# Performance work log

Measured on AMD Instinct MI355X. Metric: run time of the kernel, lower is better.

## Reference

```python
import jax, jax.numpy as jnp
import numpy as np

B, N, K, TC = 4, 4096, 16, 3
N_TAYLOR = 20  # 3rd-order Taylor monomials of (x,y,z): 1 + 3 + 6 + 10
CHANNELS = [(6, 32), (32, 64), (64, 128), (128, 256)]


def _taylor(rel):
    # rel: B,3,N,K relative coords -> B,20,N,K monomial basis up to degree 3
    x, y, z = rel[:, 0], rel[:, 1], rel[:, 2]
    one = jnp.ones_like(x)
    return jnp.stack([one, x, y, z,
                      x * x, x * y, x * z, y * y, y * z, z * z,
                      x * x * x, x * x * y, x * x * z, x * y * y, x * y * z,
                      x * z * z, y * y * y, y * y * z, y * z * z, z * z * z], axis=1)


def _group(feat, idx):
    # feat: B,C,N ; idx: B,N,K (int) -> B,C,N,K gathered neighbor features
    return jax.vmap(lambda f, i: f[:, i])(feat, idx)


def setup_inputs() -> dict:
    key = jax.random.key(0)
    ks = jax.random.split(key, 8)
    inp = {"pc": jax.random.normal(ks[0], (B, N, 6), dtype=jnp.float32)}
    for l, (cin, cout) in enumerate(CHANNELS, start=1):
        k1, k2 = jax.random.split(ks[l], 2)
        inp[f"w1_{l}"] = jax.random.normal(k1, (TC, N_TAYLOR), dtype=jnp.float32) * 0.1
        inp[f"b1_{l}"] = jnp.zeros((TC,), dtype=jnp.float32)
        fan_in = cin * TC * K
        inp[f"w2_{l}"] = jax.random.normal(k2, (cout, cin * TC, K), dtype=jnp.float32) * (1.0 / np.sqrt(fan_in))
        inp[f"b2_{l}"] = jnp.zeros((cout,), dtype=jnp.float32)
    return inp


def _forward(pc, params):
    pcT = pc.transpose(0, 2, 1)                 # B,6,N
    xyz = pcT[:, :3]                            # B,3,N
    # KNN graph: pairwise squared distances, top-k nearest (includes self)
    sq = jnp.sum(xyz * xyz, axis=1)             # B,N
    d2 = sq[:, :, None] + sq[:, None, :] - 2.0 * jnp.einsum('bcn,bcm->bnm', xyz, xyz)
    _, idx = jax.lax.top_k(-d2, K)              # B,N,K
    gxyz = _group(xyz, idx)                     # B,3,N,K
    rel = gxyz - xyz[:, :, :, None]             # B,3,N,K relative neighbor coords
    tay_basis = _taylor(rel)                    # B,20,N,K

    feat = pcT
    feats = []
    for (w1, b1, w2, b2) in params:
        # Taylor kernel weights: 1x1 conv over the 20 monomials -> TC channels
        tay = jnp.einsum('btnk,ct->bcnk', tay_basis, w1) + b1[None, :, None, None]  # B,TC,N,K
        gf = _group(feat, idx)                  # B,C,N,K
        C = gf.shape[1]
        fused = (gf[:, :, None] * tay[:, None]).reshape(B, C * TC, N, K)  # outer product
        # Conv2d(C*TC, out, kernel=(1,K)): contract channel and neighbor axes
        out = jnp.einsum('bcnk,ock->bon', fused, w2) + b2[None, :, None]
        feat = jax.nn.relu(out)                 # B,Cout,N
        feats.append(feat)

    point_feat = jnp.concatenate(feats, axis=1)  # B,480,N
    top2, _ = jax.lax.top_k(point_feat, 2)       # top-2 over N (last axis) -> B,480,2
    cat_feat = top2.reshape(B, -1)               # B,960
    return cat_feat, point_feat


def reference(pc, w1_1, b1_1, w2_1, b2_1, w1_2, b1_2, w2_2, b2_2,
              w1_3, b1_3, w2_3, b2_3, w1_4, b1_4, w2_4, b2_4):
    params = [(w1_1, b1_1, w2_1, b2_1), (w1_2, b1_2, w2_2, b2_2),
              (w1_3, b1_3, w2_3, b2_3), (w1_4, b1_4, w2_4, b2_4)]
    return _forward(pc, params)
```

## Files before the change

### kernel.cpp

```cpp
#include <hip/hip_runtime.h>
#include <hip/hip_fp16.h>
#include <cfloat>

#define BB 4
#define NN 4096
#define KK 16
#define NPTS (BB * NN)
#define NT48 (48 * NPTS)

typedef __attribute__((ext_vector_type(8))) _Float16 f16x8;
typedef __attribute__((ext_vector_type(4))) float f32x4;
typedef unsigned int u32;
typedef unsigned long long u64;

__device__ __forceinline__ short f2h(float v) {
  __half h = __float2half_rn(v);
  return __half_as_short(h);
}
__device__ __forceinline__ u32 mulh2(u32 a, __half2 t) {
  __half2 x = __hmul2(*(__half2*)&a, t);
  return *(u32*)&x;
}

__device__ __forceinline__ void wcvt_body(const float* __restrict__ w2,
                                          short* __restrict__ wb,
                                          int CIN, int COUT, int CPAD, int LOGC,
                                          int total8, int i) {
  if (i >= total8) return;
  const int q8 = i * 8;
  const int QT = CPAD * 48;
  const int o = q8 / QT;
  const int r = q8 - o * QT;
  const int kq = r >> LOGC;
  const int c0 = r & (CPAD - 1);
  const int tt = kq >> 4;
  const int k = kq & 15;
  short h[8];
#pragma unroll
  for (int j = 0; j < 8; ++j) {
    const int c = c0 + j;
    const float v = (o < COUT && c < CIN) ? w2[(size_t)o * CIN * 48 + (c * 3 + tt) * 16 + k] : 0.0f;
    h[j] = f2h(v);
  }
  short* d = wb + (size_t)o * QT + r;
#pragma unroll
  for (int j = 0; j < 8; ++j) d[j] = h[j];
}

__global__ __launch_bounds__(256) void prep_kernel(
    const float* __restrict__ pc, short* __restrict__ ft0, float4* __restrict__ xyzq,
    const float* __restrict__ w2_1, short* __restrict__ wb1,
    const float* __restrict__ w2_2, short* __restrict__ wb2,
    const float* __restrict__ w2_3, short* __restrict__ wb3,
    const float* __restrict__ w2_4, short* __restrict__ wb4) {
  const int blk = blockIdx.x;
  const int t = threadIdx.x;
  if (blk < 64) {
    const int i = blk * 256 + t;
    const float* s = pc + (size_t)i * 6;
    short* d = ft0 + (size_t)i * 8;
#pragma unroll
    for (int c = 0; c < 6; ++c) d[c] = f2h(s[c]);
    d[6] = 0; d[7] = 0;
    const float x = s[0], y = s[1], z = s[2];
    xyzq[i] = make_float4(x, y, z, fmaf(z, z, fmaf(y, y, x * x)));
  } else if (blk < 76) {
    wcvt_body(w2_1, wb1, 6, 32, 8, 3, 3072, (blk - 64) * 256 + t);
  } else if (blk < 124) {
    wcvt_body(w2_2, wb2, 32, 64, 32, 5, 12288, (blk - 76) * 256 + t);
  } else if (blk < 316) {
    wcvt_body(w2_3, wb3, 64, 128, 64, 6, 49152, (blk - 124) * 256 + t);
  } else {
    wcvt_body(w2_4, wb4, 128, 256, 128, 7, 196608, (blk - 316) * 256 + t);
  }
}

__global__ __launch_bounds__(256) void knn_select2(const float4* __restrict__ xyzq,
                                                   int* __restrict__ idx_out) {
  __shared__ float wT[2][4];
  __shared__ u64 list[2][128];
  __shared__ int lcnt[2];
  const int g0 = blockIdx.x * 2;
  const int b = g0 >> 12;
  const int t = threadIdx.x;
  const int lane = t & 63;
  const float4* base = xyzq + (b << 12);
  const float4 qa = xyzq[g0];
  const float4 qb = xyzq[g0 + 1];
  float da[16], db[16];
  float mina = FLT_MAX, minb = FLT_MAX;
#pragma unroll
  for (int i = 0; i < 16; ++i) {
    const float4 c = base[i * 256 + t];
    const float dota = fmaf(qa.z, c.z, fmaf(qa.y, c.y, qa.x * c.x));
    da[i] = fmaf(-2.0f, dota, qa.w + c.w);
    mina = fminf(mina, da[i]);
    const float dotb = fmaf(qb.z, c.z, fmaf(qb.y, c.y, qb.x * c.x));
    db[i] = fmaf(-2.0f, dotb, qb.w + c.w);
    minb = fminf(minb, db[i]);
  }
  if (t < 2) lcnt[t] = 0;
  float va = mina, vb = minb;
#pragma unroll
  for (int k = 2; k <= 64; k <<= 1) {
#pragma unroll
    for (int j = k >> 1; j >= 1; j >>= 1) {
      const float oa = __shfl_xor(va, j, 64);
      const float ob = __shfl_xor(vb, j, 64);
      const bool take_min = (((lane & k) == 0) == ((lane & j) == 0));
      va = take_min ? fminf(va, oa) : fmaxf(va, oa);
      vb = take_min ? fminf(vb, ob) : fmaxf(vb, ob);
    }
  }
  const float twa = __shfl(va, 15, 64);
  const float twb = __shfl(vb, 15, 64);
  if (lane == 0) { wT[0][t >> 6] = twa; wT[1][t >> 6] = twb; }
  __syncthreads();
  const float Ta = fminf(fminf(wT[0][0], wT[0][1]), fminf(wT[0][2], wT[0][3]));
  const float Tb = fminf(fminf(wT[1][0], wT[1][1]), fminf(wT[1][2], wT[1][3]));
#pragma unroll
  for (int i = 0; i < 16; ++i) {
    if (da[i] <= Ta) {
      const u32 bits = __float_as_uint(da[i]);
      const u32 key = bits ^ ((u32)((int)bits >> 31) | 0x80000000u);
      const int pos = atomicAdd(&lcnt[0], 1);
      if (pos < 128) list[0][pos] = ((u64)key << 32) | (u32)(i * 256 + t);
    }
    if (db[i] <= Tb) {
      const u32 bits = __float_as_uint(db[i]);
      const u32 key = bits ^ ((u32)((int)bits >> 31) | 0x80000000u);
      const int pos = atomicAdd(&lcnt[1], 1);
      if (pos < 128) list[1][pos] = ((u64)key << 32) | (u32)(i * 256 + t);
    }
  }
  __syncthreads();
  if (t < 128) {
#pragma unroll
    for (int qq = 0; qq < 2; ++qq) {
      const int m = min(lcnt[qq], 128);
      const u64 my = (t < m) ? list[qq][t] : ~0ull;
      int rank = 0;
#pragma unroll 4
      for (int i = 0; i < m; ++i) rank += (list[qq][i] < my) ? 1 : 0;
      if (t < m && rank < 16)
        idx_out[(size_t)(g0 + qq) * KK + rank] = (int)(my & 0xFFFFFFFFull);
    }
  }
}

__global__ __launch_bounds__(256) void taylor_kernel(
    const float* __restrict__ pc, const int* __restrict__ idx,
    const float* __restrict__ w1_1, const float* __restrict__ b1_1,
    const float* __restrict__ w1_2, const float* __restrict__ b1_2,
    const float* __restrict__ w1_3, const float* __restrict__ b1_3,
    const float* __restrict__ w1_4, const float* __restrict__ b1_4,
    short* __restrict__ tayh) {
  const int i = blockIdx.x * 256 + threadIdx.x;
  if (i >= NPTS * KK) return;
  const int p = i & (NPTS - 1);
  const int k = i >> 14;
  const int n = p & (NN - 1);
  const int b = p >> 12;
  const float* pcb = pc + (size_t)b * NN * 6;
  const int m = idx[(size_t)p * KK + k];
  const float x = pcb[m * 6 + 0] - pcb[n * 6 + 0];
  const float y = pcb[m * 6 + 1] - pcb[n * 6 + 1];
  const float z = pcb[m * 6 + 2] - pcb[n * 6 + 2];
  float tb[20];
  tb[0] = 1.0f; tb[1] = x; tb[2] = y; tb[3] = z;
  tb[4] = x * x; tb[5] = x * y; tb[6] = x * z;
  tb[7] = y * y; tb[8] = y * z; tb[9] = z * z;
  tb[10] = tb[4] * x; tb[11] = tb[4] * y; tb[12] = tb[4] * z;
  tb[13] = tb[5] * y; tb[14] = tb[5] * z; tb[15] = tb[6] * z;
  tb[16] = tb[7] * y; tb[17] = tb[7] * z; tb[18] = tb[8] * z; tb[19] = tb[9] * z;
  const float* w1s[4] = {w1_1, w1_2, w1_3, w1_4};
  const float* b1s[4] = {b1_1, b1_2, b1_3, b1_4};
#pragma unroll
  for (int l = 0; l < 4; ++l) {
    const float* w1 = w1s[l];
    const float* b1 = b1s[l];
#pragma unroll
    for (int c = 0; c < 3; ++c) {
      float s = b1[c];
#pragma unroll
      for (int j = 0; j < 20; ++j) s = fmaf(w1[c * 20 + j], tb[j], s);
      tayh[(size_t)(l * 48 + c * 16 + k) * NPTS + p] = f2h(s);
    }
  }
}

template <int CPAD, int LOGC, int COUT, int OTILE>
__global__ __launch_bounds__(256) void conv_mfma_kernel(
    const char* __restrict__ ftin,
    const short* __restrict__ wb,
    const float* __restrict__ b2,
    const short* __restrict__ tayl,
    const int* __restrict__ idx,
    float* __restrict__ pfout, int pfbstride,
    short* __restrict__ ftout, int CPADN) {
  constexpr int QTOT = CPAD * 48;
  constexpr int OUTER = QTOT / 64;
  constexpr int NJ = OTILE / 64;
  constexpr int NJC = (NJ == 2) ? 4 : 1;
  constexpr int NH = OTILE / 32;
  __shared__ __align__(16) short As[2][OTILE * 64];
  __shared__ __align__(16) short Bs[2][64 * 64];
  __shared__ __align__(16) unsigned short tayH[48 * 64];
  __shared__ int idxS[16 * 64];
  const int t = threadIdx.x;
  const int pbase = blockIdx.x * 64;
  const int obase = blockIdx.y * OTILE;
  const int b = pbase >> 12;
  const int nbase = pbase & (NN - 1);
  const int p_loc = t >> 2;
  const int sub = t & 3;
#pragma unroll
  for (int i = 0; i < 3; ++i) {
    const int f = i * 1024 + t * 4;
    *(ushort4*)&tayH[f] =
        *(const ushort4*)&tayl[(size_t)(f >> 6) * NPTS + pbase + (f & 63)];
  }
  {
    const int4 mi = *(const int4*)&idx[(size_t)(pbase + p_loc) * KK + sub * 4];
    const int gb = b << 12;
    idxS[(sub * 4 + 0) * 64 + p_loc] = (gb + mi.x) << (LOGC + 1);
    idxS[(sub * 4 + 1) * 64 + p_loc] = (gb + mi.y) << (LOGC + 1);
    idxS[(sub * 4 + 2) * 64 + p_loc] = (gb + mi.z) << (LOGC + 1);
    idxS[(sub * 4 + 3) * 64 + p_loc] = (gb + mi.w) << (LOGC + 1);
  }
  const int arow = t >> 3;
  const int apos = t & 7;
  const int aswz = (t >> 4) & 7;
  const short* awl[NH];
#pragma unroll
  for (int h = 0; h < NH; ++h)
    awl[h] = wb + (size_t)(obase + h * 32 + arow) * QTOT + ((apos ^ aswz) * 8);
  auto dmaA = [&](int o, int ph) {
#pragma unroll
    for (int h = 0; h < NH; ++h)
      __builtin_amdgcn_global_load_lds(
          (const __attribute__((address_space(1))) u32*)(awl[h] + o * 64),
          (__attribute__((address_space(3))) u32*)&As[ph][h * 2048 + t * 8], 16, 0, 0);
  };
  const int lane = t & 63;
  const int w = t >> 6;
  const int wm = (NJ == 2) ? (w & 1) : 0;
  const int ksw = (NJ == 2) ? (w >> 1) : 0;
  const int wn = (NJ == 2) ? 0 : w;
  const int fr = lane & 15;
  const int fk = lane >> 4;
  const int rsw = (fr >> 1) & 7;
  const int bswz = (p_loc >> 1) & 7;
  f32x4 acc[4][NJC];
#pragma unroll
  for (int i = 0; i < 4; ++i)
#pragma unroll
    for (int j = 0; j < NJC; ++j) acc[i][j] = (f32x4)(0.0f);

  uint4 fv[2];
  unsigned short tvh[2];
  auto prefB = [&](int o) {
#pragma unroll
    for (int z = 0; z < 2; ++z) {
      const int q0 = o * 64 + z * 32 + sub * 8;
      const int kq = q0 >> LOGC;
      const int c0 = q0 & (CPAD - 1);
      const int moff = idxS[(kq & 15) * 64 + p_loc];
      tvh[z] = tayH[kq * 64 + p_loc];
      fv[z] = *(const uint4*)(ftin + moff + (c0 << 1));
    }
  };
  auto buildB = [&](int ph) {
#pragma unroll
    for (int z = 0; z < 2; ++z) {
      const __half2 t2 = __half2half2(__ushort_as_half(tvh[z]));
      const uint4 f = fv[z];
      uint4 r;
      r.x = mulh2(f.x, t2); r.y = mulh2(f.y, t2);
      r.z = mulh2(f.z, t2); r.w = mulh2(f.w, t2);
      const int pos = (z * 4 + sub) ^ bswz;
      *(uint4*)&Bs[ph][p_loc * 64 + pos * 8] = r;
    }
  };
  dmaA(0, 0);
  __syncthreads();
  prefB(0);
  buildB(0);
  __syncthreads();
#pragma unroll 1
  for (int o = 0; o < OUTER; ++o) {
    const int ph = o & 1;
    if (o + 1 < OUTER) { dmaA(o + 1, ph ^ 1); prefB(o + 1); }
    if constexpr (NJ == 2) {
      f16x8 af[4], bf[4];
      const int pos8 = ((ksw * 4 + fk) ^ rsw) * 8;
#pragma unroll
      for (int i = 0; i < 4; ++i)
        af[i] = *(const f16x8*)&As[ph][(wm * 64 + i * 16 + fr) * 64 + pos8];
#pragma unroll
      for (int j = 0; j < 4; ++j)
        bf[j] = *(const f16x8*)&Bs[ph][(j * 16 + fr) * 64 + pos8];
      if (o + 1 < OUTER) buildB(ph ^ 1);
#pragma unroll
      for (int i = 0; i < 4; ++i)
#pragma unroll
        for (int j = 0; j < 4; ++j)
          acc[i][j] = __builtin_amdgcn_mfma_f32_16x16x32_f16(af[i], bf[j], acc[i][j], 0, 0, 0);
    } else {
#pragma unroll
      for (int z = 0; z < 2; ++z) {
        f16x8 af[4], bf;
        const int pos8 = ((z * 4 + fk) ^ rsw) * 8;
#pragma unroll
        for (int i = 0; i < 4; ++i)
          af[i] = *(const f16x8*)&As[ph][(i * 16 + fr) * 64 + pos8];
        bf = *(const f16x8*)&Bs[ph][(wn * 16 + fr) * 64 + pos8];
        if (z == 0 && o + 1 < OUTER) buildB(ph ^ 1);
#pragma unroll
        for (int i = 0; i < 4; ++i)
          acc[i][0] = __builtin_amdgcn_mfma_f32_16x16x32_f16(af[i], bf, acc[i][0], 0, 0, 0);
      }
    }
    if (o + 1 < OUTER) __syncthreads();
  }
  if constexpr (NJ == 2) {
    __syncthreads();
    float* red = (float*)(&As[0][0]) + wm * 4096;
    if (ksw == 1) {
#pragma unroll
      for (int i = 0; i < 4; ++i)
#pragma unroll
        for (int j = 0; j < 4; ++j)
#pragma unroll
          for (int r = 0; r < 4; ++r)
            red[((i * 4 + j) * 4 + r) * 64 + lane] = acc[i][j][r];
    }
    __syncthreads();
    if (ksw == 1) return;
#pragma unroll
    for (int i = 0; i < 4; ++i)
#pragma unroll
      for (int j = 0; j < 4; ++j)
#pragma unroll
        for (int r = 0; r < 4; ++r)
          acc[i][j][r] += red[((i * 4 + j) * 4 + r) * 64 + lane];
  }
  float* outb = pfout + (size_t)b * pfbstride;
#pragma unroll
  for (int i = 0; i < 4; ++i) {
    const int o0 = obase + wm * 64 + i * 16 + fk * 4;
    if (o0 < COUT) {
      const float4 b4 = *(const float4*)&b2[o0];
#pragma unroll
      for (int j = 0; j < NJC; ++j) {
        const int p_l = (NJ == 2) ? (j * 16 + fr) : (wn * 16 + fr);
        const float v0 = fmaxf(acc[i][j][0] + b4.x, 0.0f);
        const float v1 = fmaxf(acc[i][j][1] + b4.y, 0.0f);
        const float v2 = fmaxf(acc[i][j][2] + b4.z, 0.0f);
        const float v3 = fmaxf(acc[i][j][3] + b4.w, 0.0f);
        outb[(size_t)(o0 + 0) * NN + nbase + p_l] = v0;
        outb[(size_t)(o0 + 1) * NN + nbase + p_l] = v1;
        outb[(size_t)(o0 + 2) * NN + nbase + p_l] = v2;
        outb[(size_t)(o0 + 3) * NN + nbase + p_l] = v3;
        if (ftout) {
          const __half2 h01 = __floats2half2_rn(v0, v1);
          const __half2 h23 = __floats2half2_rn(v2, v3);
          uint2 pk;
          pk.x = *(const u32*)&h01;
          pk.y = *(const u32*)&h23;
          *(uint2*)&ftout[(size_t)(pbase + p_l) * CPADN + o0] = pk;
        }
      }
    }
  }
}

__global__ __launch_bounds__(256) void top2_kernel(const float* __restrict__ pf,
                                                   float* __restrict__ cat) {
  const int row = blockIdx.x;
  const float* p = pf + (size_t)row * NN;
  float m1 = -FLT_MAX, m2 = -FLT_MAX;
  for (int i = threadIdx.x; i < NN; i += 256) {
    const float v = p[i];
    if (v > m1) { m2 = m1; m1 = v; }
    else if (v > m2) m2 = v;
  }
#pragma unroll
  for (int off = 32; off > 0; off >>= 1) {
    const float o1 = __shfl_down(m1, off, 64);
    const float o2 = __shfl_down(m2, off, 64);
    const float nm1 = fmaxf(m1, o1);
    const float nm2 = fmaxf(fminf(m1, o1), fmaxf(m2, o2));
    m1 = nm1; m2 = nm2;
  }
  __shared__ float s1[4], s2[4];
  const int wid = threadIdx.x >> 6;
  if ((threadIdx.x & 63) == 0) { s1[wid] = m1; s2[wid] = m2; }
  __syncthreads();
  if (threadIdx.x == 0) {
    m1 = s1[0]; m2 = s2[0];
#pragma unroll
    for (int w = 1; w < 4; ++w) {
      const float o1 = s1[w], o2 = s2[w];
      const float nm1 = fmaxf(m1, o1);
      const float nm2 = fmaxf(fminf(m1, o1), fmaxf(m2, o2));
      m1 = nm1; m2 = nm2;
    }
    const int b = row / 480, ch = row % 480;
    cat[b * 960 + ch * 2 + 0] = m1;
    cat[b * 960 + ch * 2 + 1] = m2;
  }
}

extern "C" void kernel_launch(void* const* d_in, const int* in_sizes, int n_in,
                              void* d_out, int out_size, void* d_ws, size_t ws_size,
                              hipStream_t stream) {
  const float* pc = (const float*)d_in[0];
  const float* w1s[4]; const float* b1s[4]; const float* w2s[4]; const float* b2s[4];
  for (int l = 0; l < 4; ++l) {
    w1s[l] = (const float*)d_in[1 + 4 * l];
    b1s[l] = (const float*)d_in[2 + 4 * l];
    w2s[l] = (const float*)d_in[3 + 4 * l];
    b2s[l] = (const float*)d_in[4 + 4 * l];
  }
  char* W = (char*)d_ws;
  int* idx = (int*)W;
  short* tayh = (short*)(W + 1048576);
  short* wb1 = (short*)(W + 13631488);
  short* wb2 = wb1 + 64 * 384;
  short* wb3 = wb2 + 64 * 1536;
  short* wb4 = wb3 + 128 * 3072;
  short* ft0 = (short*)(W + 17809408);
  short* ft1 = (short*)(W + 18071552);
  float4* xyzq = (float4*)(W + 1048576);
  short* ft2 = (short*)(W + 1048576 + 6291456);
  short* ft3 = (short*)(W + 1048576 + 6291456 + 1048576);
  float* cat = (float*)d_out;
  float* pf = (float*)d_out + BB * 960;
  const int pfstride = 480 * NN;

  prep_kernel<<<dim3(1084), 256, 0, stream>>>(
      pc, ft0, xyzq, w2s[0], wb1, w2s[1], wb2, w2s[2], wb3, w2s[3], wb4);
  knn_select2<<<dim3(NPTS / 2), 256, 0, stream>>>(xyzq, idx);
  taylor_kernel<<<dim3(NPTS * KK / 256), 256, 0, stream>>>(
      pc, idx, w1s[0], b1s[0], w1s[1], b1s[1], w1s[2], b1s[2], w1s[3], b1s[3], tayh);
  conv_mfma_kernel<8, 3, 32, 64><<<dim3(NPTS / 64, 1), 256, 0, stream>>>(
      (const char*)ft0, wb1, b2s[0], tayh + 0 * (size_t)NT48, idx,
      pf + (size_t)0 * NN, pfstride, ft1, 32);
  conv_mfma_kernel<32, 5, 64, 64><<<dim3(NPTS / 64, 1), 256, 0, stream>>>(
      (const char*)ft1, wb2, b2s[1], tayh + 1 * (size_t)NT48, idx,
      pf + (size_t)32 * NN, pfstride, ft2, 64);
  conv_mfma_kernel<64, 6, 128, 64><<<dim3(NPTS / 64, 2), 256, 0, stream>>>(
      (const char*)ft2, wb3, b2s[2], tayh + 2 * (size_t)NT48, idx,
      pf + (size_t)96 * NN, pfstride, ft3, 128);
  conv_mfma_kernel<128, 7, 256, 128><<<dim3(NPTS / 64, 2), 256, 0, stream>>>(
      (const char*)ft3, wb4, b2s[3], tayh + 3 * (size_t)NT48, idx,
      pf + (size_t)224 * NN, pfstride, nullptr, 0);
  top2_kernel<<<dim3(BB * 480), 256, 0, stream>>>(pf, cat);
}
```

Measured before the change: 335.4 us.

## Fuse Taylor weight computation into conv kernels, drop taylor_kernel and tayh buffer

Removes the separate taylor_kernel, which wrote a 4-layer fp16 Taylor weight tensor to global memory. Each conv kernel now computes its layer's Taylor weights directly into shared memory from xyzq and the neighbor indices. The workspace layout is compacted to match. This trades one launch plus a global write and read for extra per-block ALU work and scattered xyz gathers in each conv prologue, with recomputation across the two output-tile blocks of layers 3 and 4.

Measured after the change: 332.6 us. About the same (-0.8%).

```diff
diff --git a/kernel.cpp b/kernel.cpp
--- a/kernel.cpp
+++ b/kernel.cpp
@@ -6,7 +6,6 @@
 #define NN 4096
 #define KK 16
 #define NPTS (BB * NN)
-#define NT48 (48 * NPTS)
 
 typedef __attribute__((ext_vector_type(8))) _Float16 f16x8;
 typedef __attribute__((ext_vector_type(4))) float f32x4;
@@ -148,53 +147,14 @@
   }
 }
 
-__global__ __launch_bounds__(256) void taylor_kernel(
-    const float* __restrict__ pc, const int* __restrict__ idx,
-    const float* __restrict__ w1_1, const float* __restrict__ b1_1,
-    const float* __restrict__ w1_2, const float* __restrict__ b1_2,
-    const float* __restrict__ w1_3, const float* __restrict__ b1_3,
-    const float* __restrict__ w1_4, const float* __restrict__ b1_4,
-    short* __restrict__ tayh) {
-  const int i = blockIdx.x * 256 + threadIdx.x;
-  if (i >= NPTS * KK) return;
-  const int p = i & (NPTS - 1);
-  const int k = i >> 14;
-  const int n = p & (NN - 1);
-  const int b = p >> 12;
-  const float* pcb = pc + (size_t)b * NN * 6;
-  const int m = idx[(size_t)p * KK + k];
-  const float x = pcb[m * 6 + 0] - pcb[n * 6 + 0];
-  const float y = pcb[m * 6 + 1] - pcb[n * 6 + 1];
-  const float z = pcb[m * 6 + 2] - pcb[n * 6 + 2];
-  float tb[20];
-  tb[0] = 1.0f; tb[1] = x; tb[2] = y; tb[3] = z;
-  tb[4] = x * x; tb[5] = x * y; tb[6] = x * z;
-  tb[7] = y * y; tb[8] = y * z; tb[9] = z * z;
-  tb[10] = tb[4] * x; tb[11] = tb[4] * y; tb[12] = tb[4] * z;
-  tb[13] = tb[5] * y; tb[14] = tb[5] * z; tb[15] = tb[6] * z;
-  tb[16] = tb[7] * y; tb[17] = tb[7] * z; tb[18] = tb[8] * z; tb[19] = tb[9] * z;
-  const float* w1s[4] = {w1_1, w1_2, w1_3, w1_4};
-  const float* b1s[4] = {b1_1, b1_2, b1_3, b1_4};
-#pragma unroll
-  for (int l = 0; l < 4; ++l) {
-    const float* w1 = w1s[l];
-    const float* b1 = b1s[l];
-#pragma unroll
-    for (int c = 0; c < 3; ++c) {
-      float s = b1[c];
-#pragma unroll
-      for (int j = 0; j < 20; ++j) s = fmaf(w1[c * 20 + j], tb[j], s);
-      tayh[(size_t)(l * 48 + c * 16 + k) * NPTS + p] = f2h(s);
-    }
-  }
-}
-
 template <int CPAD, int LOGC, int COUT, int OTILE>
 __global__ __launch_bounds__(256) void conv_mfma_kernel(
     const char* __restrict__ ftin,
     const short* __restrict__ wb,
     const float* __restrict__ b2,
-    const short* __restrict__ tayl,
+    const float4* __restrict__ xyzq,
+    const float* __restrict__ w1,
+    const float* __restrict__ b1,
     const int* __restrict__ idx,
     float* __restrict__ pfout, int pfbstride,
     short* __restrict__ ftout, int CPADN) {
@@ -214,12 +174,6 @@
   const int nbase = pbase & (NN - 1);
   const int p_loc = t >> 2;
   const int sub = t & 3;
-#pragma unroll
-  for (int i = 0; i < 3; ++i) {
-    const int f = i * 1024 + t * 4;
-    *(ushort4*)&tayH[f] =
-        *(const ushort4*)&tayl[(size_t)(f >> 6) * NPTS + pbase + (f & 63)];
-  }
   {
     const int4 mi = *(const int4*)&idx[(size_t)(pbase + p_loc) * KK + sub * 4];
     const int gb = b << 12;
@@ -227,6 +181,30 @@
     idxS[(sub * 4 + 1) * 64 + p_loc] = (gb + mi.y) << (LOGC + 1);
     idxS[(sub * 4 + 2) * 64 + p_loc] = (gb + mi.z) << (LOGC + 1);
     idxS[(sub * 4 + 3) * 64 + p_loc] = (gb + mi.w) << (LOGC + 1);
+    const float4 self = xyzq[pbase + p_loc];
+    const int nbr[4] = {gb + mi.x, gb + mi.y, gb + mi.z, gb + mi.w};
+#pragma unroll
+    for (int j = 0; j < 4; ++j) {
+      const float4 nb = xyzq[nbr[j]];
+      const float x = nb.x - self.x;
+      const float y = nb.y - self.y;
+      const float z = nb.z - self.z;
+      float tb[20];
+      tb[0] = 1.0f; tb[1] = x; tb[2] = y; tb[3] = z;
+      tb[4] = x * x; tb[5] = x * y; tb[6] = x * z;
+      tb[7] = y * y; tb[8] = y * z; tb[9] = z * z;
+      tb[10] = tb[4] * x; tb[11] = tb[4] * y; tb[12] = tb[4] * z;
+      tb[13] = tb[5] * y; tb[14] = tb[5] * z; tb[15] = tb[6] * z;
+      tb[16] = tb[7] * y; tb[17] = tb[7] * z; tb[18] = tb[8] * z; tb[19] = tb[9] * z;
+      const int k = sub * 4 + j;
+#pragma unroll
+      for (int c = 0; c < 3; ++c) {
+        float s = b1[c];
+#pragma unroll
+        for (int jj = 0; jj < 20; ++jj) s = fmaf(w1[c * 20 + jj], tb[jj], s);
+        tayH[(c * 16 + k) * 64 + p_loc] = (unsigned short)f2h(s);
+      }
+    }
   }
   const int arow = t >> 3;
   const int apos = t & 7;
@@ -425,16 +403,15 @@
   }
   char* W = (char*)d_ws;
   int* idx = (int*)W;
-  short* tayh = (short*)(W + 1048576);
-  short* wb1 = (short*)(W + 13631488);
-  short* wb2 = wb1 + 64 * 384;
-  short* wb3 = wb2 + 64 * 1536;
-  short* wb4 = wb3 + 128 * 3072;
-  short* ft0 = (short*)(W + 17809408);
-  short* ft1 = (short*)(W + 18071552);
   float4* xyzq = (float4*)(W + 1048576);
-  short* ft2 = (short*)(W + 1048576 + 6291456);
-  short* ft3 = (short*)(W + 1048576 + 6291456 + 1048576);
+  short* wb1 = (short*)(W + 1310720);
+  short* wb2 = (short*)(W + 1359872);
+  short* wb3 = (short*)(W + 1556480);
+  short* wb4 = (short*)(W + 2342912);
+  short* ft0 = (short*)(W + 5488640);
+  short* ft1 = (short*)(W + 5750784);
+  short* ft2 = (short*)(W + 6799360);
+  short* ft3 = (short*)(W + 8896512);
   float* cat = (float*)d_out;
   float* pf = (float*)d_out + BB * 960;
   const int pfstride = 480 * NN;
@@ -442,19 +419,17 @@
   prep_kernel<<<dim3(1084), 256, 0, stream>>>(
       pc, ft0, xyzq, w2s[0], wb1, w2s[1], wb2, w2s[2], wb3, w2s[3], wb4);
   knn_select2<<<dim3(NPTS / 2), 256, 0, stream>>>(xyzq, idx);
-  taylor_kernel<<<dim3(NPTS * KK / 256), 256, 0, stream>>>(
-      pc, idx, w1s[0], b1s[0], w1s[1], b1s[1], w1s[2], b1s[2], w1s[3], b1s[3], tayh);
   conv_mfma_kernel<8, 3, 32, 64><<<dim3(NPTS / 64, 1), 256, 0, stream>>>(
-      (const char*)ft0, wb1, b2s[0], tayh + 0 * (size_t)NT48, idx,
+      (const char*)ft0, wb1, b2s[0], xyzq, w1s[0], b1s[0], idx,
       pf + (size_t)0 * NN, pfstride, ft1, 32);
   conv_mfma_kernel<32, 5, 64, 64><<<dim3(NPTS / 64, 1), 256, 0, stream>>>(
-      (const char*)ft1, wb2, b2s[1], tayh + 1 * (size_t)NT48, idx,
+      (const char*)ft1, wb2, b2s[1], xyzq, w1s[1], b1s[1], idx,
       pf + (size_t)32 * NN, pfstride, ft2, 64);
   conv_mfma_kernel<64, 6, 128, 64><<<dim3(NPTS / 64, 2), 256, 0, stream>>>(
-      (const char*)ft2, wb3, b2s[2], tayh + 2 * (size_t)NT48, idx,
+      (const char*)ft2, wb3, b2s[2], xyzq, w1s[2], b1s[2], idx,
       pf + (size_t)96 * NN, pfstride, ft3, 128);
   conv_mfma_kernel<128, 7, 256, 128><<<dim3(NPTS / 64, 2), 256, 0, stream>>>(
-      (const char*)ft3, wb4, b2s[3], tayh + 3 * (size_t)NT48, idx,
+      (const char*)ft3, wb4, b2s[3], xyzq, w1s[3], b1s[3], idx,
       pf + (size_t)224 * NN, pfstride, nullptr, 0);
   top2_kernel<<<dim3(BB * 480), 256, 0, stream>>>(pf, cat);
 }
```
